# Optimization experiments

Hardware: AMD Instinct MI355X
Metric: run time of the kernel (lower is better)

The kernel has to match this reference:

```python
import jax, jax.numpy as jnp
import numpy as np

B, N, D, C, NCLS = 8, 2048, 256, 128, 50
EPS = 1e-5  # BatchNorm eps

def _bn(x, g, b):
    # eval-mode BatchNorm1d over channel dim of (B,C,N): running_mean=0, running_var=1
    return x * (g / jnp.sqrt(1.0 + EPS))[:, None] + b[:, None]

def _complex_linear(x, Wr, br, Wi, bi):
    # torch ComplexLinear: complex(fr(x.real)-fi(x.imag), fr(x.imag)+fi(x.real))
    xr, xi = x.real, x.imag
    re = (xr @ Wr.T + br) - (xi @ Wi.T + bi)
    im = (xi @ Wr.T + br) + (xr @ Wi.T + bi)
    return jax.lax.complex(re, im)

def _sa(x, qkW, vW, vb, tW, tb, g, b):
    # x: (B,C,N); q/k share weights (tied in torch), dim C//4
    xq = jnp.einsum('qc,bcn->bnq', qkW, x)            # (B,N,C/4)
    xk = jnp.einsum('qc,bcm->bqm', qkW, x)            # (B,C/4,N)
    energy = jnp.einsum('bnq,bqm->bnm', xq, xk)       # (B,N,N)
    attn = jax.nn.softmax(energy, axis=-1)
    attn = attn / (1e-9 + attn.sum(axis=1, keepdims=True))  # column renorm
    xv = jnp.einsum('oc,bcn->bon', vW, x) + vb[:, None]
    xr = x - jnp.einsum('bcn,bnm->bcm', xv, attn)
    xr = jnp.einsum('oc,bcn->bon', tW, xr) + tb[:, None]
    return x + jax.nn.relu(_bn(xr, g, b))

def reference(xyz, cls_label, A, Bmat, W1r, b1r, W1i, b1i, W2r, b2r, W2i, b2i,
              lbl_emb, ft_w1, ft_g1, ft_b1, ft_w2, ft_g2, ft_b2,
              sa_qk, sa_vw, sa_vb, sa_tw, sa_tb, sa_g, sa_b,
              fuse_w, fuse_g, fuse_b, c1_w, c1_b, bn1_g, bn1_b, c2_w, c2_b):
    pts = xyz.transpose(0, 2, 1)                       # (B,N,3)
    # VecKM(d=256, alpha=30, beta=9): G = eB (eB^H eA), normalized to sqrt(d)
    eA = jnp.exp(1j * (pts @ A))                       # (B,N,D) complex64
    eB = jnp.exp(1j * (pts @ Bmat))
    inner = jnp.einsum('bnd,bne->bde', eB.conj(), eA)  # (B,D,D)
    G = jnp.einsum('bnd,bde->bne', eB, inner)          # (B,N,D)
    G = G / jnp.linalg.norm(G, axis=-1, keepdims=True) * jnp.sqrt(jnp.float32(D))
    G = _complex_linear(G, W1r, b1r, W1i, b1i)
    G = jax.lax.complex(jax.nn.relu(G.real), jax.nn.relu(G.imag))  # ComplexReLU
    G = _complex_linear(G, W2r, b2r, W2i, b2i)
    G = (G.real ** 2 + G.imag ** 2).transpose(0, 2, 1)  # (B,D,N)
    reweight = (cls_label @ lbl_emb)[:, :, None]        # (B,D,1)
    x = G * reweight
    x = jax.nn.relu(_bn(jnp.einsum('oc,bcn->bon', ft_w1, x), ft_g1, ft_b1))
    x = _bn(jnp.einsum('oc,bcn->bon', ft_w2, x), ft_g2, ft_b2)  # (B,C,N)
    feats = []
    for i in range(4):
        x = _sa(x, sa_qk[i], sa_vw[i], sa_vb[i], sa_tw[i], sa_tb[i], sa_g[i], sa_b[i])
        feats.append(x)
    x = jnp.concatenate(feats, axis=1)                  # (B,4C,N)
    x = jax.nn.relu(_bn(jnp.einsum('oc,bcn->bon', fuse_w, x), fuse_g, fuse_b))
    x = jax.nn.relu(_bn(jnp.einsum('oc,bcn->bon', c1_w, x) + c1_b[:, None], bn1_g, bn1_b))
    # dropout is identity in eval mode
    x = jnp.einsum('oc,bcn->bon', c2_w, x) + c2_b[:, None]
    x = jax.nn.log_softmax(x, axis=1)
    return x.transpose(0, 2, 1)                         # (B,N,NCLS)

def setup_inputs():
    key = jax.random.key(0)
    k = jax.random.split(key, 24)
    rn = lambda i, s: jax.random.normal(k[i], s, jnp.float32)
    s = 0.05
    return {
        'xyz': rn(0, (B, 3, N)),
        'cls_label': jax.random.uniform(k[1], (B, 16), jnp.float32),
        'A': rn(2, (3, D)) * 30.0,
        'Bmat': rn(3, (3, D)) * 9.0,
        'W1r': rn(4, (D, D)) * s, 'b1r': rn(5, (D,)) * s,
        'W1i': rn(6, (D, D)) * s, 'b1i': rn(7, (D,)) * s,
        'W2r': rn(8, (D, D)) * s, 'b2r': rn(9, (D,)) * s,
        'W2i': rn(10, (D, D)) * s, 'b2i': rn(11, (D,)) * s,
        'lbl_emb': rn(12, (16, D)),
        'ft_w1': rn(13, (C, D)) * s, 'ft_g1': jnp.ones((C,)), 'ft_b1': jnp.zeros((C,)),
        'ft_w2': rn(14, (C, C)) * s, 'ft_g2': jnp.ones((C,)), 'ft_b2': jnp.zeros((C,)),
        'sa_qk': rn(15, (4, C // 4, C)) * s,
        'sa_vw': rn(16, (4, C, C)) * s, 'sa_vb': rn(17, (4, C)) * s,
        'sa_tw': rn(18, (4, C, C)) * s, 'sa_tb': rn(19, (4, C)) * s,
        'sa_g': jnp.ones((4, C)), 'sa_b': jnp.zeros((4, C)),
        'fuse_w': rn(20, (C, 4 * C)) * s, 'fuse_g': jnp.ones((C,)), 'fuse_b': jnp.zeros((C,)),
        'c1_w': rn(21, (C, C)) * s, 'c1_b': rn(22, (C,)) * s,
        'bn1_g': jnp.ones((C,)), 'bn1_b': jnp.zeros((C,)),
        'c2_w': rn(23, (NCLS, C)) * s, 'c2_b': jnp.zeros((NCLS,)),
    }
```

## Files before the change

### kernel.cpp

```cpp
#include <hip/hip_runtime.h>

#define BB 8
#define NPTS 2048
#define DD 256
#define CCH 128
#define NCLASS 50
#define LOG2E 1.4426950408889634f

typedef __attribute__((ext_vector_type(8))) short short8;
typedef __attribute__((ext_vector_type(4))) float f32x4;
typedef unsigned short u16;
#define MFMA16(a,b,c) __builtin_amdgcn_mfma_f32_16x16x32_bf16(a,b,c,0,0,0)

__device__ __forceinline__ u16 f2bf(float x){
  union { float f; unsigned int u; } v; v.f = x;
  unsigned int r = v.u + 0x7FFFu + ((v.u >> 16) & 1u);
  return (u16)(r >> 16);
}
__device__ __forceinline__ float bf2f(u16 u){
  union { unsigned int u32; float f; } v; v.u32 = ((unsigned int)u) << 16; return v.f;
}
__device__ __forceinline__ void split2(float x, u16& h, u16& l){
  h = f2bf(x); l = f2bf(x - bf2f(h));
}
__device__ __forceinline__ short8 ld8(const u16* p){ return *(const short8*)p; }
__device__ __forceinline__ short8 zero8(){ short8 z = {0,0,0,0,0,0,0,0}; return z; }

struct WSplit {
  const float* src[12];
  int cnt[12];
  int off[12];
};
__global__ __launch_bounds__(256) void wsplit_kernel(WSplit wsp, u16* __restrict__ H,
                                                     u16* __restrict__ L)
{
  int seg = blockIdx.y;
  int idx = blockIdx.x*256 + threadIdx.x;
  if (idx >= wsp.cnt[seg]) return;
  float v = wsp.src[seg][idx];
  u16 h, l; split2(v, h, l);
  H[wsp.off[seg]+idx] = h; L[wsp.off[seg]+idx] = l;
}

__global__ __launch_bounds__(256) void ek1_kernel(
    const float* __restrict__ xyz, const float* __restrict__ A, const float* __restrict__ Bm,
    u16* __restrict__ ATrh, u16* __restrict__ ATrl, u16* __restrict__ ATih, u16* __restrict__ ATil,
    u16* __restrict__ BTrh, u16* __restrict__ BTrl, u16* __restrict__ BTih, u16* __restrict__ BTil)
{
  size_t idx = (size_t)blockIdx.x*256 + threadIdx.x;
  int n = (int)(idx & (NPTS-1));
  int d = (int)((idx >> 11) & (DD-1));
  int b = (int)(idx >> 19);
  float p0 = xyz[((size_t)b*3+0)*NPTS+n];
  float p1 = xyz[((size_t)b*3+1)*NPTS+n];
  float p2 = xyz[((size_t)b*3+2)*NPTS+n];
  float phA = p0*A[d] + p1*A[DD+d] + p2*A[2*DD+d];
  float phB = p0*Bm[d] + p1*Bm[DD+d] + p2*Bm[2*DD+d];
  float sa, ca, sb, cb;
  sincosf(phA, &sa, &ca);
  sincosf(phB, &sb, &cb);
  size_t off = ((size_t)b*DD + d)*NPTS + n;
  u16 h, l;
  split2(ca, h, l); ATrh[off] = h; ATrl[off] = l;
  split2(sa, h, l); ATih[off] = h; ATil[off] = l;
  split2(cb, h, l); BTrh[off] = h; BTrl[off] = l;
  split2(sb, h, l); BTih[off] = h; BTil[off] = l;
}

__global__ __launch_bounds__(256) void ek2_kernel(
    const float* __restrict__ xyz, const float* __restrict__ Bm,
    u16* __restrict__ Brh, u16* __restrict__ Brl, u16* __restrict__ Bih, u16* __restrict__ Bil)
{
  size_t idx = (size_t)blockIdx.x*256 + threadIdx.x;
  int d = (int)(idx & (DD-1));
  int n = (int)((idx >> 8) & (NPTS-1));
  int b = (int)(idx >> 19);
  float p0 = xyz[((size_t)b*3+0)*NPTS+n];
  float p1 = xyz[((size_t)b*3+1)*NPTS+n];
  float p2 = xyz[((size_t)b*3+2)*NPTS+n];
  float phB = p0*Bm[d] + p1*Bm[DD+d] + p2*Bm[2*DD+d];
  float sb, cb;
  sincosf(phB, &sb, &cb);
  size_t off = ((size_t)b*NPTS + n)*DD + d;
  u16 h, l;
  split2(cb, h, l); Brh[off] = h; Brl[off] = l;
  split2(sb, h, l); Bih[off] = h; Bil[off] = l;
}

__global__ __launch_bounds__(256) void inner_mfma_kernel(
    const u16* __restrict__ ATrh, const u16* __restrict__ ATrl,
    const u16* __restrict__ ATih, const u16* __restrict__ ATil,
    const u16* __restrict__ BTrh, const u16* __restrict__ BTrl,
    const u16* __restrict__ BTih, const u16* __restrict__ BTil,
    float2* __restrict__ PART)
{
  int z = blockIdx.z; int b = z & 7; int ch = z >> 3;
  int e0 = blockIdx.y*64, d0 = blockIdx.x*64;
  int tid = threadIdx.x, lane = tid & 63, w = tid >> 6;
  int wr = (w >> 1)*32, wc = (w & 1)*32;
  int r16 = lane & 15, g4 = lane >> 4;
  f32x4 re[2][2] = {}, ip[2][2] = {}, iq[2][2] = {};
  size_t ar_[2], br_[2];
  #pragma unroll
  for (int rg = 0; rg < 2; rg++) {
    ar_[rg] = ((size_t)b*DD + (e0 + wr + rg*16 + r16))*NPTS + g4*8;
    br_[rg] = ((size_t)b*DD + (d0 + wc + rg*16 + r16))*NPTS + g4*8;
  }
  int kbeg = ch*512;
  #pragma unroll 2
  for (int kk = 0; kk < 512; kk += 32) {
    int k0 = kbeg + kk;
    short8 arh[2], arl[2], aih[2], ail[2], brh[2], brl[2], bih[2], bil[2];
    #pragma unroll
    for (int rg = 0; rg < 2; rg++) {
      arh[rg] = ld8(ATrh + ar_[rg] + k0); arl[rg] = ld8(ATrl + ar_[rg] + k0);
      aih[rg] = ld8(ATih + ar_[rg] + k0); ail[rg] = ld8(ATil + ar_[rg] + k0);
      brh[rg] = ld8(BTrh + br_[rg] + k0); brl[rg] = ld8(BTrl + br_[rg] + k0);
      bih[rg] = ld8(BTih + br_[rg] + k0); bil[rg] = ld8(BTil + br_[rg] + k0);
    }
    #pragma unroll
    for (int ra = 0; ra < 2; ra++)
      #pragma unroll
      for (int rb = 0; rb < 2; rb++) {
        re[ra][rb] = MFMA16(arh[ra], brh[rb], re[ra][rb]);
        re[ra][rb] = MFMA16(arh[ra], brl[rb], re[ra][rb]);
        re[ra][rb] = MFMA16(arl[ra], brh[rb], re[ra][rb]);
        re[ra][rb] = MFMA16(aih[ra], bih[rb], re[ra][rb]);
        re[ra][rb] = MFMA16(aih[ra], bil[rb], re[ra][rb]);
        re[ra][rb] = MFMA16(ail[ra], bih[rb], re[ra][rb]);
        ip[ra][rb] = MFMA16(aih[ra], brh[rb], ip[ra][rb]);
        ip[ra][rb] = MFMA16(aih[ra], brl[rb], ip[ra][rb]);
        ip[ra][rb] = MFMA16(ail[ra], brh[rb], ip[ra][rb]);
        iq[ra][rb] = MFMA16(arh[ra], bih[rb], iq[ra][rb]);
        iq[ra][rb] = MFMA16(arh[ra], bil[rb], iq[ra][rb]);
        iq[ra][rb] = MFMA16(arl[ra], bih[rb], iq[ra][rb]);
      }
  }
  float2* outp = PART + ((size_t)(ch*BB + b)*DD)*DD;
  #pragma unroll
  for (int ra = 0; ra < 2; ra++)
    #pragma unroll
    for (int rb = 0; rb < 2; rb++)
      #pragma unroll
      for (int j = 0; j < 4; j++) {
        int e = e0 + wr + ra*16 + g4*4 + j;
        int d = d0 + wc + rb*16 + r16;
        outp[(size_t)e*DD + d] = make_float2(re[ra][rb][j], ip[ra][rb][j] - iq[ra][rb][j]);
      }
}

__global__ __launch_bounds__(256) void innred_kernel(const float2* __restrict__ P,
    u16* __restrict__ Irh, u16* __restrict__ Irl, u16* __restrict__ Iih, u16* __restrict__ Iil)
{
  size_t i = (size_t)blockIdx.x*256 + threadIdx.x;
  const size_t S = (size_t)BB*DD*DD;
  float2 a = P[i], b = P[i+S], c = P[i+2*S], d = P[i+3*S];
  float rr = a.x+b.x+c.x+d.x, ii = a.y+b.y+c.y+d.y;
  u16 h, l;
  split2(rr, h, l); Irh[i] = h; Irl[i] = l;
  split2(ii, h, l); Iih[i] = h; Iil[i] = l;
}

__global__ __launch_bounds__(256) void g_mfma_kernel(
    const u16* __restrict__ Brh, const u16* __restrict__ Brl,
    const u16* __restrict__ Bih, const u16* __restrict__ Bil,
    const u16* __restrict__ Irh, const u16* __restrict__ Irl,
    const u16* __restrict__ Iih, const u16* __restrict__ Iil,
    float2* __restrict__ G)
{
  int b = blockIdx.z;
  int n0 = blockIdx.y*64, e0 = blockIdx.x*64;
  int tid = threadIdx.x, lane = tid & 63, w = tid >> 6;
  int wr = (w >> 1)*32, wc = (w & 1)*32;
  int r16 = lane & 15, g4 = lane >> 4;
  f32x4 p[2][2] = {}, q[2][2] = {}, im[2][2] = {};
  size_t ar_[2], br_[2];
  #pragma unroll
  for (int rg = 0; rg < 2; rg++) {
    ar_[rg] = ((size_t)b*NPTS + (n0 + wr + rg*16 + r16))*DD + g4*8;
    br_[rg] = ((size_t)b*DD + (e0 + wc + rg*16 + r16))*DD + g4*8;
  }
  #pragma unroll
  for (int k0 = 0; k0 < DD; k0 += 32) {
    short8 arh[2], arl[2], aih[2], ail[2], brh[2], brl[2], bih[2], bil[2];
    #pragma unroll
    for (int rg = 0; rg < 2; rg++) {
      arh[rg] = ld8(Brh + ar_[rg] + k0); arl[rg] = ld8(Brl + ar_[rg] + k0);
      aih[rg] = ld8(Bih + ar_[rg] + k0); ail[rg] = ld8(Bil + ar_[rg] + k0);
      brh[rg] = ld8(Irh + br_[rg] + k0); brl[rg] = ld8(Irl + br_[rg] + k0);
      bih[rg] = ld8(Iih + br_[rg] + k0); bil[rg] = ld8(Iil + br_[rg] + k0);
    }
    #pragma unroll
    for (int ra = 0; ra < 2; ra++)
      #pragma unroll
      for (int rb = 0; rb < 2; rb++) {
        p[ra][rb] = MFMA16(arh[ra], brh[rb], p[ra][rb]);
        p[ra][rb] = MFMA16(arh[ra], brl[rb], p[ra][rb]);
        p[ra][rb] = MFMA16(arl[ra], brh[rb], p[ra][rb]);
        q[ra][rb] = MFMA16(aih[ra], bih[rb], q[ra][rb]);
        q[ra][rb] = MFMA16(aih[ra], bil[rb], q[ra][rb]);
        q[ra][rb] = MFMA16(ail[ra], bih[rb], q[ra][rb]);
        im[ra][rb] = MFMA16(arh[ra], bih[rb], im[ra][rb]);
        im[ra][rb] = MFMA16(arh[ra], bil[rb], im[ra][rb]);
        im[ra][rb] = MFMA16(arl[ra], bih[rb], im[ra][rb]);
        im[ra][rb] = MFMA16(aih[ra], brh[rb], im[ra][rb]);
        im[ra][rb] = MFMA16(aih[ra], brl[rb], im[ra][rb]);
        im[ra][rb] = MFMA16(ail[ra], brh[rb], im[ra][rb]);
      }
  }
  #pragma unroll
  for (int ra = 0; ra < 2; ra++)
    #pragma unroll
    for (int rb = 0; rb < 2; rb++)
      #pragma unroll
      for (int j = 0; j < 4; j++) {
        int n = n0 + wr + ra*16 + g4*4 + j;
        int e = e0 + wc + rb*16 + r16;
        G[((size_t)b*NPTS + n)*DD + e] = make_float2(p[ra][rb][j] - q[ra][rb][j], im[ra][rb][j]);
      }
}

__global__ __launch_bounds__(256) void gnormsplit_kernel(const float2* __restrict__ Gf,
    u16* __restrict__ Grh, u16* __restrict__ Grl, u16* __restrict__ Gih, u16* __restrict__ Gil)
{
  size_t row = blockIdx.x;
  const float2* p = Gf + row*DD;
  int tid = threadIdx.x;
  float2 v = p[tid];
  __shared__ float red[256];
  red[tid] = v.x*v.x + v.y*v.y;
  __syncthreads();
  for (int w = 128; w > 0; w >>= 1) { if (tid < w) red[tid] += red[tid+w]; __syncthreads(); }
  float sc = 16.f * rsqrtf(red[0]);
  size_t off = row*DD + tid;
  u16 h, l;
  split2(v.x*sc, h, l); Grh[off] = h; Grl[off] = l;
  split2(v.y*sc, h, l); Gih[off] = h; Gil[off] = l;
}

__global__ __launch_bounds__(256) void clinear_mfma_kernel(
    const u16* __restrict__ Arh, const u16* __restrict__ Arl,
    const u16* __restrict__ Aih, const u16* __restrict__ Ail,
    const u16* __restrict__ Wrh, const u16* __restrict__ Wrl,
    const u16* __restrict__ Wih, const u16* __restrict__ Wil,
    const float* __restrict__ br, const float* __restrict__ bi,
    u16* __restrict__ Orh, u16* __restrict__ Orl, u16* __restrict__ Oih, u16* __restrict__ Oil,
    const float* __restrict__ RW, float* __restrict__ GSQ, int mode)
{
  int wg = blockIdx.y * gridDim.x + blockIdx.x;
  int xcd = wg & 7, idx = wg >> 3;
  int o0 = (idx & 3) * 64;
  int m0 = (xcd * ((int)gridDim.y >> 3) + (idx >> 2)) * 64;
  int tid = threadIdx.x, lane = tid & 63, w = tid >> 6;
  int wr = (w >> 1)*32, wc = (w & 1)*32;
  int r16 = lane & 15, g4 = lane >> 4;
  f32x4 p[2][2] = {}, q[2][2] = {}, im[2][2] = {};
  size_t ar_[2], br_[2];
  #pragma unroll
  for (int rg = 0; rg < 2; rg++) {
    ar_[rg] = (size_t)(m0 + wr + rg*16 + r16)*DD + g4*8;
    br_[rg] = (size_t)(o0 + wc + rg*16 + r16)*DD + g4*8;
  }
  #pragma unroll
  for (int k0 = 0; k0 < DD; k0 += 32) {
    short8 arh[2], arl[2], aih[2], ail[2], brh[2], brl[2], bih[2], bil[2];
    #pragma unroll
    for (int rg = 0; rg < 2; rg++) {
      arh[rg] = ld8(Arh + ar_[rg] + k0); arl[rg] = ld8(Arl + ar_[rg] + k0);
      aih[rg] = ld8(Aih + ar_[rg] + k0); ail[rg] = ld8(Ail + ar_[rg] + k0);
      brh[rg] = ld8(Wrh + br_[rg] + k0); brl[rg] = ld8(Wrl + br_[rg] + k0);
      bih[rg] = ld8(Wih + br_[rg] + k0); bil[rg] = ld8(Wil + br_[rg] + k0);
    }
    #pragma unroll
    for (int ra = 0; ra < 2; ra++)
      #pragma unroll
      for (int rb = 0; rb < 2; rb++) {
        p[ra][rb] = MFMA16(arh[ra], brh[rb], p[ra][rb]);
        p[ra][rb] = MFMA16(arh[ra], brl[rb], p[ra][rb]);
        p[ra][rb] = MFMA16(arl[ra], brh[rb], p[ra][rb]);
        q[ra][rb] = MFMA16(aih[ra], bih[rb], q[ra][rb]);
        q[ra][rb] = MFMA16(aih[ra], bil[rb], q[ra][rb]);
        q[ra][rb] = MFMA16(ail[ra], bih[rb], q[ra][rb]);
        im[ra][rb] = MFMA16(arh[ra], bih[rb], im[ra][rb]);
        im[ra][rb] = MFMA16(arh[ra], bil[rb], im[ra][rb]);
        im[ra][rb] = MFMA16(arl[ra], bih[rb], im[ra][rb]);
        im[ra][rb] = MFMA16(aih[ra], brh[rb], im[ra][rb]);
        im[ra][rb] = MFMA16(aih[ra], brl[rb], im[ra][rb]);
        im[ra][rb] = MFMA16(ail[ra], brh[rb], im[ra][rb]);
      }
  }
  #pragma unroll
  for (int ra = 0; ra < 2; ra++)
    #pragma unroll
    for (int rb = 0; rb < 2; rb++) {
      int o = o0 + wc + rb*16 + r16;
      float brv = br[o], biv = bi[o];
      if (mode == 1) {
        #pragma unroll
        for (int j = 0; j < 4; j++) {
          int m = m0 + wr + ra*16 + g4*4 + j;
          float re = fmaxf(p[ra][rb][j] - q[ra][rb][j] + brv - biv, 0.f);
          float iv = fmaxf(im[ra][rb][j] + brv + biv, 0.f);
          size_t off = (size_t)m*DD + o;
          u16 h, l;
          split2(re, h, l); Orh[off] = h; Orl[off] = l;
          split2(iv, h, l); Oih[off] = h; Oil[off] = l;
        }
      } else {
        int mbase = m0 + wr + ra*16 + g4*4;
        int b = mbase >> 11, nb = mbase & (NPTS-1);
        float rwv = RW[(size_t)b*DD + o];
        float4 gv;
        #pragma unroll
        for (int j = 0; j < 4; j++) {
          float re = p[ra][rb][j] - q[ra][rb][j] + brv - biv;
          float iv = im[ra][rb][j] + brv + biv;
          ((float*)&gv)[j] = (re*re + iv*iv) * rwv;
        }
        *(float4*)(GSQ + ((size_t)b*DD + o)*NPTS + nb) = gv;
      }
    }
}

__global__ void rw_kernel(const float* __restrict__ cls, const float* __restrict__ lbl,
                          float* __restrict__ RW)
{
  int b = blockIdx.x; int d = threadIdx.x;
  float s = 0.f;
  #pragma unroll
  for (int k = 0; k < 16; k++) s += cls[b*16+k] * lbl[k*DD+d];
  RW[b*DD+d] = s;
}

__global__ __launch_bounds__(256) void sgemm_kernel(
    const u16* __restrict__ Wh, const u16* __restrict__ Wl,
    const float* __restrict__ X, float* __restrict__ Y,
    const float* __restrict__ RES,
    const float* __restrict__ bias, const float* __restrict__ bng, const float* __restrict__ bnb,
    u16* __restrict__ YBh, u16* __restrict__ YBl, int ybmode,
    int O, int Cin, size_t xbs, size_t ybs, size_t rbs, int flags)
{
  int b = blockIdx.z;
  int n0 = blockIdx.x*64, o0 = blockIdx.y*64;
  const float* x = X + (size_t)b*xbs;
  __shared__ u16 sXh[64][40], sXl[64][40];
  int tid = threadIdx.x, lane = tid & 63, w = tid >> 6;
  int wo = (w >> 1)*32, wn = (w & 1)*32;
  int r16 = lane & 15, g4 = lane >> 4;
  f32x4 acc[2][2] = {};
  int stc = tid >> 3;
  int stn = (tid & 7)*8;
  for (int k0 = 0; k0 < Cin; k0 += 32) {
    const float* px = x + (size_t)(k0+stc)*NPTS + n0 + stn;
    float4 u0 = *(const float4*)px;
    float4 u1 = *(const float4*)(px+4);
    float v[8] = {u0.x,u0.y,u0.z,u0.w,u1.x,u1.y,u1.z,u1.w};
    __syncthreads();
    #pragma unroll
    for (int j = 0; j < 8; j++) {
      u16 h, l; split2(v[j], h, l);
      sXh[stn+j][stc] = h; sXl[stn+j][stc] = l;
    }
    __syncthreads();
    short8 awh[2], awl[2], bxh[2], bxl[2];
    #pragma unroll
    for (int rg = 0; rg < 2; rg++) {
      int orow = o0 + wo + rg*16 + r16;
      if (orow < O) {
        size_t woff = (size_t)orow*Cin + k0 + g4*8;
        awh[rg] = ld8(Wh + woff); awl[rg] = ld8(Wl + woff);
      } else { awh[rg] = zero8(); awl[rg] = zero8(); }
      bxh[rg] = ld8(&sXh[wn + rg*16 + r16][g4*8]);
      bxl[rg] = ld8(&sXl[wn + rg*16 + r16][g4*8]);
    }
    #pragma unroll
    for (int ra = 0; ra < 2; ra++)
      #pragma unroll
      for (int rb = 0; rb < 2; rb++) {
        acc[ra][rb] = MFMA16(awh[ra], bxh[rb], acc[ra][rb]);
        acc[ra][rb] = MFMA16(awh[ra], bxl[rb], acc[ra][rb]);
        acc[ra][rb] = MFMA16(awl[ra], bxh[rb], acc[ra][rb]);
      }
  }
  #pragma unroll
  for (int ra = 0; ra < 2; ra++)
    #pragma unroll
    for (int rb = 0; rb < 2; rb++)
      #pragma unroll
      for (int j = 0; j < 4; j++) {
        int o = o0 + wo + ra*16 + g4*4 + j;
        if (o >= O) continue;
        int n = n0 + wn + rb*16 + r16;
        float v = acc[ra][rb][j];
        if (flags & 1) v += bias[o];
        if (flags & 2) v = v * (bng[o] * rsqrtf(1.f + 1e-5f)) + bnb[o];
        if (flags & 4) v = fmaxf(v, 0.f);
        if (flags & 8) v += RES[(size_t)b*rbs + (size_t)o*NPTS + n];
        if (ybmode == 0) Y[(size_t)b*ybs + (size_t)o*NPTS + n] = v;
        else if (ybmode == 1) YBh[(size_t)b*ybs + (size_t)o*NPTS + n] = f2bf(v);
        else {
          u16 h, l; split2(v, h, l);
          size_t off = ((size_t)b*NPTS + n)*32 + o;
          YBh[off] = h; YBl[off] = l;
        }
      }
}

__global__ __launch_bounds__(256) void sastat_kernel(
    const u16* __restrict__ Qh, const u16* __restrict__ Ql,
    float* __restrict__ PM, float* __restrict__ PS)
{
  int b = blockIdx.z, ch = blockIdx.y;
  int n0 = blockIdx.x*64;
  size_t base = (size_t)b*NPTS*32;
  int tid = threadIdx.x, lane = tid & 63, wid = tid >> 6;
  int r16 = lane & 15, g4 = lane >> 4;
  size_t ao = base + (size_t)(n0 + wid*16 + r16)*32 + g4*8;
  short8 ah = ld8(Qh + ao), al = ld8(Ql + ao);
  float pm[4] = {-3.4e38f,-3.4e38f,-3.4e38f,-3.4e38f};
  float ps[4] = {0.f,0.f,0.f,0.f};
  int mbeg = ch*512, mend = mbeg + 512;
  for (int mt = mbeg; mt < mend; mt += 32) {
    size_t bo0 = base + (size_t)(mt + r16)*32 + g4*8;
    size_t bo1 = bo0 + 16*32;
    short8 bh0 = ld8(Qh+bo0), bl0 = ld8(Ql+bo0);
    short8 bh1 = ld8(Qh+bo1), bl1 = ld8(Ql+bo1);
    f32x4 a0 = {}, a1 = {};
    a0 = MFMA16(ah, bh0, a0); a0 = MFMA16(ah, bl0, a0); a0 = MFMA16(al, bh0, a0);
    a1 = MFMA16(ah, bh1, a1); a1 = MFMA16(ah, bl1, a1); a1 = MFMA16(al, bh1, a1);
    #pragma unroll
    for (int j = 0; j < 4; j++) {
      float v = fmaxf(a0[j], a1[j]);
      float mn = fmaxf(pm[j], v);
      ps[j] = ps[j]*exp2f((pm[j]-mn)*LOG2E)
            + exp2f((a0[j]-mn)*LOG2E) + exp2f((a1[j]-mn)*LOG2E);
      pm[j] = mn;
    }
  }
  #pragma unroll
  for (int j = 0; j < 4; j++) {
    float m = pm[j], s = ps[j];
    #pragma unroll
    for (int d = 1; d < 16; d <<= 1) {
      float om = __shfl_xor(m, d);
      float os = __shfl_xor(s, d);
      float mn = fmaxf(m, om);
      s = s*exp2f((m-mn)*LOG2E) + os*exp2f((om-mn)*LOG2E);
      m = mn;
    }
    if (r16 == 0) {
      int n_ = n0 + wid*16 + g4*4 + j;
      size_t off = ((size_t)ch*BB + b)*NPTS + n_;
      PM[off] = m; PS[off] = s;
    }
  }
}

__global__ __launch_bounds__(256) void comb1_kernel(
    const float* __restrict__ PM, const float* __restrict__ PS,
    float* __restrict__ MX, float* __restrict__ RS)
{
  size_t i = (size_t)blockIdx.x*256 + threadIdx.x;
  const size_t S = (size_t)BB*NPTS;
  float m0 = PM[i], m1 = PM[i+S], m2 = PM[i+2*S], m3 = PM[i+3*S];
  float mx = fmaxf(fmaxf(m0,m1), fmaxf(m2,m3));
  float den = PS[i]*exp2f((m0-mx)*LOG2E) + PS[i+S]*exp2f((m1-mx)*LOG2E)
            + PS[i+2*S]*exp2f((m2-mx)*LOG2E) + PS[i+3*S]*exp2f((m3-mx)*LOG2E);
  MX[i] = mx; RS[i] = 1.f/den;
}

__global__ __launch_bounds__(512) void fused_pv_kernel(
    const u16* __restrict__ Qh, const u16* __restrict__ Ql,
    const float* __restrict__ MX, const float* __restrict__ RS,
    const u16* __restrict__ XV, const float* __restrict__ XRES, size_t res_bs,
    float* __restrict__ OUT)
{
  int b = blockIdx.y;
  int m0 = blockIdx.x*64;
  size_t qbase = (size_t)b*NPTS*32;
  const u16* xv = XV + (size_t)b*CCH*NPTS;
  __shared__ float smx[NPTS], srs[NPTS];
  __shared__ u16 Pl[64][36];
  __shared__ float csacc[64];
  int tid = threadIdx.x, lane = tid & 63, w = tid >> 6;
  int r16 = lane & 15, g4 = lane >> 4;
  for (int t = tid; t < NPTS; t += 512) {
    smx[t] = MX[(size_t)b*NPTS + t];
    srs[t] = RS[(size_t)b*NPTS + t];
  }
  if (tid < 64) csacc[tid] = 0.f;
  int ma = w >> 1, na = w & 1;
  int cw = (w >> 1)*32, mw = (w & 1)*32;
  size_t eao = qbase + (size_t)(m0 + ma*16 + r16)*32 + g4*8;
  short8 eah = ld8(Qh + eao), eal = ld8(Ql + eao);
  const u16* pa0 = xv + (size_t)(cw + r16)*NPTS + g4*8;
  const u16* pa1 = pa0 + (size_t)16*NPTS;
  f32x4 acc[2][2] = {};
  float cs[4] = {0.f,0.f,0.f,0.f};
  size_t ebo = qbase + (size_t)(na*16 + r16)*32 + g4*8;
  short8 ebh = ld8(Qh + ebo), ebl = ld8(Ql + ebo);
  short8 xa0 = ld8(pa0), xa1 = ld8(pa1);
  __syncthreads();
  for (int nt = 0; nt < NPTS; nt += 32) {
    f32x4 e = {};
    e = MFMA16(eah, ebh, e); e = MFMA16(eah, ebl, e); e = MFMA16(eal, ebh, e);
    int nn = nt + na*16 + r16;
    float mxv_ = smx[nn], rsv_ = srs[nn];
    #pragma unroll
    for (int j = 0; j < 4; j++) {
      float t = exp2f((e[j]-mxv_)*LOG2E)*rsv_;
      cs[j] += t;
      Pl[ma*16 + g4*4 + j][na*16 + r16] = f2bf(t);
    }
    short8 nebh = zero8(), nebl = zero8(), nxa0 = zero8(), nxa1 = zero8();
    if (nt + 32 < NPTS) {
      size_t ebo2 = qbase + (size_t)(nt + 32 + na*16 + r16)*32 + g4*8;
      nebh = ld8(Qh + ebo2); nebl = ld8(Ql + ebo2);
      nxa0 = ld8(pa0 + nt + 32); nxa1 = ld8(pa1 + nt + 32);
    }
    __syncthreads();
    short8 b0 = *(const short8*)&Pl[mw + r16][g4*8];
    short8 b1 = *(const short8*)&Pl[mw + 16 + r16][g4*8];
    acc[0][0] = MFMA16(xa0, b0, acc[0][0]);
    acc[0][1] = MFMA16(xa0, b1, acc[0][1]);
    acc[1][0] = MFMA16(xa1, b0, acc[1][0]);
    acc[1][1] = MFMA16(xa1, b1, acc[1][1]);
    __syncthreads();
    ebh = nebh; ebl = nebl; xa0 = nxa0; xa1 = nxa1;
  }
  #pragma unroll
  for (int j = 0; j < 4; j++) {
    float c = cs[j];
    #pragma unroll
    for (int d = 1; d < 16; d <<= 1) c += __shfl_xor(c, d);
    if (r16 == 0) atomicAdd(&csacc[ma*16 + g4*4 + j], c);
  }
  __syncthreads();
  #pragma unroll
  for (int ca = 0; ca < 2; ca++)
    #pragma unroll
    for (int mb = 0; mb < 2; mb++) {
      int m = m0 + mw + mb*16 + r16;
      float ci = 1.f/(1e-9f + csacc[mw + mb*16 + r16]);
      #pragma unroll
      for (int j = 0; j < 4; j++) {
        int c = cw + ca*16 + g4*4 + j;
        float v = XRES[(size_t)b*res_bs + (size_t)c*NPTS + m] - acc[ca][mb][j]*ci;
        OUT[((size_t)b*CCH + c)*NPTS + m] = v;
      }
    }
}

__global__ __launch_bounds__(256) void lsm_kernel(const float* __restrict__ Y,
                                                  float* __restrict__ OUT)
{
  int idx = blockIdx.x*256 + threadIdx.x;
  int b = idx >> 11, n = idx & (NPTS-1);
  const float* p = Y + (size_t)b*NCLASS*NPTS + n;
  float m = -3.4e38f;
  #pragma unroll
  for (int k = 0; k < NCLASS; k++) m = fmaxf(m, p[(size_t)k*NPTS]);
  float s = 0.f;
  #pragma unroll
  for (int k = 0; k < NCLASS; k++) s += expf(p[(size_t)k*NPTS] - m);
  float L = m + logf(s);
  float* o = OUT + (size_t)idx*NCLASS;
  #pragma unroll
  for (int k = 0; k < NCLASS; k++) o[k] = p[(size_t)k*NPTS] - L;
}

extern "C" void kernel_launch(void* const* d_in, const int* in_sizes, int n_in,
                              void* d_out, int out_size, void* d_ws, size_t ws_size,
                              hipStream_t stream)
{
  (void)in_sizes; (void)n_in; (void)out_size; (void)ws_size;
  const float* xyz  = (const float*)d_in[0];
  const float* cls  = (const float*)d_in[1];
  const float* Amat = (const float*)d_in[2];
  const float* Bm   = (const float*)d_in[3];
  const float* W1r  = (const float*)d_in[4];
  const float* b1r  = (const float*)d_in[5];
  const float* W1i  = (const float*)d_in[6];
  const float* b1i  = (const float*)d_in[7];
  const float* W2r  = (const float*)d_in[8];
  const float* b2r  = (const float*)d_in[9];
  const float* W2i  = (const float*)d_in[10];
  const float* b2i  = (const float*)d_in[11];
  const float* lbl  = (const float*)d_in[12];
  const float* ftw1 = (const float*)d_in[13];
  const float* ftg1 = (const float*)d_in[14];
  const float* ftb1 = (const float*)d_in[15];
  const float* ftw2 = (const float*)d_in[16];
  const float* ftg2 = (const float*)d_in[17];
  const float* ftb2 = (const float*)d_in[18];
  const float* saqk = (const float*)d_in[19];
  const float* savw = (const float*)d_in[20];
  const float* savb = (const float*)d_in[21];
  const float* satw = (const float*)d_in[22];
  const float* satb = (const float*)d_in[23];
  const float* sag  = (const float*)d_in[24];
  const float* sab  = (const float*)d_in[25];
  const float* fusew= (const float*)d_in[26];
  const float* fuseg= (const float*)d_in[27];
  const float* fuseb= (const float*)d_in[28];
  const float* c1w  = (const float*)d_in[29];
  const float* c1b  = (const float*)d_in[30];
  const float* bn1g = (const float*)d_in[31];
  const float* bn1b = (const float*)d_in[32];
  const float* c2w  = (const float*)d_in[33];
  const float* c2b  = (const float*)d_in[34];
  float* out = (float*)d_out;

  float* ws = (float*)d_ws;
  const size_t PS  = (size_t)BB*DD*NPTS;
  const size_t ISZ = (size_t)BB*DD*DD;
  u16* U = (u16*)ws;
  u16 *ATrh = U+0*PS, *ATrl = U+1*PS, *ATih = U+2*PS, *ATil = U+3*PS;
  u16 *BTrh = U+4*PS, *BTrl = U+5*PS, *BTih = U+6*PS, *BTil = U+7*PS;
  u16 *Bnrh = U+8*PS, *Bnrl = U+9*PS, *Bnih = U+10*PS, *Bnil = U+11*PS;
  u16 *Irh = U+12*PS, *Irl = U+12*PS+ISZ, *Iih = U+12*PS+2*ISZ, *Iil = U+12*PS+3*ISZ;
  float* gsq = (float*)(U + 12*PS + 4*ISZ);
  float2* PART = (float2*)gsq;
  float2* Gf = (float2*)ws;
  u16 *G1rh = U+4*PS, *G1rl = U+5*PS, *G1ih = U+6*PS, *G1il = U+7*PS;
  u16 *G2rh = U+8*PS, *G2rl = U+9*PS, *G2ih = U+10*PS, *G2il = U+11*PS;
  size_t p = (size_t)BB*NPTS*NPTS;
  float* xfeat = ws + p;  p += (size_t)BB*CCH*NPTS;
  float* feats = ws + p;  p += (size_t)BB*4*CCH*NPTS;
  float* xt1   = ws + p;  p += (size_t)BB*CCH*NPTS;
  float* xt2   = ws + p;  p += (size_t)BB*CCH*NPTS;
  float* ybuf  = ws + p;  p += (size_t)BB*NCLASS*NPTS;
  float* rwb   = ws + p;  p += (size_t)BB*DD;
  float* mxv   = ws + p;  p += (size_t)BB*NPTS;
  float* rsv   = ws + p;  p += (size_t)BB*NPTS;
  float* PMb   = ws + p;  p += (size_t)4*BB*NPTS;
  float* PSb   = ws + p;  p += (size_t)4*BB*NPTS;
  u16* xqh = (u16*)(ws + p);
  u16* xql = xqh + (size_t)BB*NPTS*32;
  u16* xvb = xql + (size_t)BB*NPTS*32;
  u16* wpH = xvb + (size_t)BB*CCH*NPTS;
  u16* wpL = wpH + 557056;

  const int o_w1r=0, o_w1i=65536, o_w2r=131072, o_w2i=196608, o_ft1=262144,
            o_ft2=294912, o_qk=311296, o_vw=327680, o_tw=393216, o_fu=458752,
            o_c1=524288, o_c2=540672;
  WSplit wsp;
  const float* srcs[12] = {W1r,W1i,W2r,W2i,ftw1,ftw2,saqk,savw,satw,fusew,c1w,c2w};
  const int cnts[12] = {65536,65536,65536,65536,32768,16384,16384,65536,65536,65536,16384,6400};
  const int offs[12] = {o_w1r,o_w1i,o_w2r,o_w2i,o_ft1,o_ft2,o_qk,o_vw,o_tw,o_fu,o_c1,o_c2};
  for (int i = 0; i < 12; i++) { wsp.src[i]=srcs[i]; wsp.cnt[i]=cnts[i]; wsp.off[i]=offs[i]; }

  wsplit_kernel<<<dim3(256, 12), 256, 0, stream>>>(wsp, wpH, wpL);
  rw_kernel<<<BB, DD, 0, stream>>>(cls, lbl, rwb);
  ek1_kernel<<<(int)(PS/256), 256, 0, stream>>>(xyz, Amat, Bm,
      ATrh, ATrl, ATih, ATil, BTrh, BTrl, BTih, BTil);
  ek2_kernel<<<(int)(PS/256), 256, 0, stream>>>(xyz, Bm, Bnrh, Bnrl, Bnih, Bnil);
  inner_mfma_kernel<<<dim3(DD/64, DD/64, BB*4), 256, 0, stream>>>(
      ATrh, ATrl, ATih, ATil, BTrh, BTrl, BTih, BTil, PART);
  innred_kernel<<<(int)(ISZ/256), 256, 0, stream>>>(PART, Irh, Irl, Iih, Iil);
  g_mfma_kernel<<<dim3(DD/64, NPTS/64, BB), 256, 0, stream>>>(
      Bnrh, Bnrl, Bnih, Bnil, Irh, Irl, Iih, Iil, Gf);
  gnormsplit_kernel<<<BB*NPTS, 256, 0, stream>>>(Gf, G1rh, G1rl, G1ih, G1il);
  clinear_mfma_kernel<<<dim3(DD/64, (BB*NPTS)/64), 256, 0, stream>>>(
      G1rh, G1rl, G1ih, G1il, wpH+o_w1r, wpL+o_w1r, wpH+o_w1i, wpL+o_w1i,
      b1r, b1i, G2rh, G2rl, G2ih, G2il, nullptr, nullptr, 1);
  clinear_mfma_kernel<<<dim3(DD/64, (BB*NPTS)/64), 256, 0, stream>>>(
      G2rh, G2rl, G2ih, G2il, wpH+o_w2r, wpL+o_w2r, wpH+o_w2i, wpL+o_w2i,
      b2r, b2i, nullptr, nullptr, nullptr, nullptr, rwb, gsq, 2);

  sgemm_kernel<<<dim3(NPTS/64, CCH/64, BB), 256, 0, stream>>>(
      wpH+o_ft1, wpL+o_ft1, gsq, xt1, nullptr, nullptr, ftg1, ftb1, nullptr, nullptr, 0,
      CCH, DD, (size_t)DD*NPTS, (size_t)CCH*NPTS, 0, 2|4);
  sgemm_kernel<<<dim3(NPTS/64, CCH/64, BB), 256, 0, stream>>>(
      wpH+o_ft2, wpL+o_ft2, xt1, xfeat, nullptr, nullptr, ftg2, ftb2, nullptr, nullptr, 0,
      CCH, CCH, (size_t)CCH*NPTS, (size_t)CCH*NPTS, 0, 2);

  const float* xsrc = xfeat;
  size_t xbs = (size_t)CCH*NPTS;
  for (int i = 0; i < 4; i++) {
    sgemm_kernel<<<dim3(NPTS/64, 1, BB), 256, 0, stream>>>(
        wpH+o_qk + i*32*CCH, wpL+o_qk + i*32*CCH, xsrc, nullptr, nullptr,
        nullptr, nullptr, nullptr, xqh, xql, 2, 32, CCH, xbs, 0, 0, 0);
    sastat_kernel<<<dim3(NPTS/64, 4, BB), 256, 0, stream>>>(xqh, xql, PMb, PSb);
    comb1_kernel<<<(BB*NPTS)/256, 256, 0, stream>>>(PMb, PSb, mxv, rsv);
    sgemm_kernel<<<dim3(NPTS/64, CCH/64, BB), 256, 0, stream>>>(
        wpH+o_vw + i*CCH*CCH, wpL+o_vw + i*CCH*CCH, xsrc, nullptr, nullptr,
        savb + i*CCH, nullptr, nullptr, xvb, nullptr, 1, CCH, CCH, xbs,
        (size_t)CCH*NPTS, 0, 1);
    fused_pv_kernel<<<dim3(NPTS/64, BB), 512, 0, stream>>>(
        xqh, xql, mxv, rsv, xvb, xsrc, xbs, xt2);
    sgemm_kernel<<<dim3(NPTS/64, CCH/64, BB), 256, 0, stream>>>(
        wpH+o_tw + i*CCH*CCH, wpL+o_tw + i*CCH*CCH, xt2, feats + (size_t)i*CCH*NPTS, xsrc,
        satb + i*CCH, sag + i*CCH, sab + i*CCH, nullptr, nullptr, 0,
        CCH, CCH, (size_t)CCH*NPTS, (size_t)4*CCH*NPTS, xbs, 1|2|4|8);
    xsrc = feats + (size_t)i*CCH*NPTS;
    xbs = (size_t)4*CCH*NPTS;
  }

  sgemm_kernel<<<dim3(NPTS/64, CCH/64, BB), 256, 0, stream>>>(
      wpH+o_fu, wpL+o_fu, feats, xt1, nullptr, nullptr, fuseg, fuseb, nullptr, nullptr, 0,
      CCH, 4*CCH, (size_t)4*CCH*NPTS, (size_t)CCH*NPTS, 0, 2|4);
  sgemm_kernel<<<dim3(NPTS/64, CCH/64, BB), 256, 0, stream>>>(
      wpH+o_c1, wpL+o_c1, xt1, xt2, nullptr, c1b, bn1g, bn1b, nullptr, nullptr, 0,
      CCH, CCH, (size_t)CCH*NPTS, (size_t)CCH*NPTS, 0, 1|2|4);
  sgemm_kernel<<<dim3(NPTS/64, 1, BB), 256, 0, stream>>>(
      wpH+o_c2, wpL+o_c2, xt2, ybuf, nullptr, c2b, nullptr, nullptr, nullptr, nullptr, 0,
      NCLASS, CCH, (size_t)CCH*NPTS, (size_t)NCLASS*NPTS, 0, 1);
  lsm_kernel<<<(BB*NPTS)/256, 256, 0, stream>>>(ybuf, out);
}
```

Baseline: 970.5 us.

## Fuse softmax partial combine into PV kernel, widen PV tile, simplify clinear grid

Removes the separate comb1 kernel by combining the four partial softmax max/sum values inside fused_pv_kernel's shared-memory preload, which saves a launch and a global round trip per SA layer. The PV inner loop now handles 64 keys per iteration instead of 32, halving the number of barriers, but it drops the register prefetch of the next Q and V tiles, so loads are issued in the same iteration that consumes them. The clinear kernel also loses its XCD-aware block swizzle in favour of plain blockIdx mapping, which may reduce L2 locality. Each PV block now recomputes the combine work that comb1 did once.

```diff
diff --git a/kernel.cpp b/kernel.cpp
--- a/kernel.cpp
+++ b/kernel.cpp
@@ -247,10 +247,7 @@
     u16* __restrict__ Orh, u16* __restrict__ Orl, u16* __restrict__ Oih, u16* __restrict__ Oil,
     const float* __restrict__ RW, float* __restrict__ GSQ, int mode)
 {
-  int wg = blockIdx.y * gridDim.x + blockIdx.x;
-  int xcd = wg & 7, idx = wg >> 3;
-  int o0 = (idx & 3) * 64;
-  int m0 = (xcd * ((int)gridDim.y >> 3) + (idx >> 2)) * 64;
+  int m0 = blockIdx.y*64, o0 = blockIdx.x*64;
   int tid = threadIdx.x, lane = tid & 63, w = tid >> 6;
   int wr = (w >> 1)*32, wc = (w & 1)*32;
   int r16 = lane & 15, g4 = lane >> 4;
@@ -456,22 +453,9 @@
   }
 }
 
-__global__ __launch_bounds__(256) void comb1_kernel(
-    const float* __restrict__ PM, const float* __restrict__ PS,
-    float* __restrict__ MX, float* __restrict__ RS)
-{
-  size_t i = (size_t)blockIdx.x*256 + threadIdx.x;
-  const size_t S = (size_t)BB*NPTS;
-  float m0 = PM[i], m1 = PM[i+S], m2 = PM[i+2*S], m3 = PM[i+3*S];
-  float mx = fmaxf(fmaxf(m0,m1), fmaxf(m2,m3));
-  float den = PS[i]*exp2f((m0-mx)*LOG2E) + PS[i+S]*exp2f((m1-mx)*LOG2E)
-            + PS[i+2*S]*exp2f((m2-mx)*LOG2E) + PS[i+3*S]*exp2f((m3-mx)*LOG2E);
-  MX[i] = mx; RS[i] = 1.f/den;
-}
-
 __global__ __launch_bounds__(512) void fused_pv_kernel(
     const u16* __restrict__ Qh, const u16* __restrict__ Ql,
-    const float* __restrict__ MX, const float* __restrict__ RS,
+    const float* __restrict__ PM, const float* __restrict__ PS,
     const u16* __restrict__ XV, const float* __restrict__ XRES, size_t res_bs,
     float* __restrict__ OUT)
 {
@@ -480,13 +464,18 @@
   size_t qbase = (size_t)b*NPTS*32;
   const u16* xv = XV + (size_t)b*CCH*NPTS;
   __shared__ float smx[NPTS], srs[NPTS];
-  __shared__ u16 Pl[64][36];
+  __shared__ u16 Pl[64][72];
   __shared__ float csacc[64];
   int tid = threadIdx.x, lane = tid & 63, w = tid >> 6;
   int r16 = lane & 15, g4 = lane >> 4;
+  const size_t S = (size_t)BB*NPTS;
   for (int t = tid; t < NPTS; t += 512) {
-    smx[t] = MX[(size_t)b*NPTS + t];
-    srs[t] = RS[(size_t)b*NPTS + t];
+    size_t bn = (size_t)b*NPTS + t;
+    float m0_ = PM[bn], m1 = PM[S+bn], m2 = PM[2*S+bn], m3 = PM[3*S+bn];
+    float mxv = fmaxf(fmaxf(m0_,m1), fmaxf(m2,m3));
+    float den = PS[bn]*exp2f((m0_-mxv)*LOG2E) + PS[S+bn]*exp2f((m1-mxv)*LOG2E)
+              + PS[2*S+bn]*exp2f((m2-mxv)*LOG2E) + PS[3*S+bn]*exp2f((m3-mxv)*LOG2E);
+    smx[t] = mxv; srs[t] = 1.f/den;
   }
   if (tid < 64) csacc[tid] = 0.f;
   int ma = w >> 1, na = w & 1;
@@ -497,36 +486,40 @@
   const u16* pa1 = pa0 + (size_t)16*NPTS;
   f32x4 acc[2][2] = {};
   float cs[4] = {0.f,0.f,0.f,0.f};
-  size_t ebo = qbase + (size_t)(na*16 + r16)*32 + g4*8;
-  short8 ebh = ld8(Qh + ebo), ebl = ld8(Ql + ebo);
-  short8 xa0 = ld8(pa0), xa1 = ld8(pa1);
   __syncthreads();
-  for (int nt = 0; nt < NPTS; nt += 32) {
-    f32x4 e = {};
-    e = MFMA16(eah, ebh, e); e = MFMA16(eah, ebl, e); e = MFMA16(eal, ebh, e);
-    int nn = nt + na*16 + r16;
-    float mxv_ = smx[nn], rsv_ = srs[nn];
-    #pragma unroll
-    for (int j = 0; j < 4; j++) {
-      float t = exp2f((e[j]-mxv_)*LOG2E)*rsv_;
-      cs[j] += t;
-      Pl[ma*16 + g4*4 + j][na*16 + r16] = f2bf(t);
-    }
-    short8 nebh = zero8(), nebl = zero8(), nxa0 = zero8(), nxa1 = zero8();
-    if (nt + 32 < NPTS) {
-      size_t ebo2 = qbase + (size_t)(nt + 32 + na*16 + r16)*32 + g4*8;
-      nebh = ld8(Qh + ebo2); nebl = ld8(Ql + ebo2);
-      nxa0 = ld8(pa0 + nt + 32); nxa1 = ld8(pa1 + nt + 32);
+  for (int nt = 0; nt < NPTS; nt += 64) {
+    #pragma unroll
+    for (int sub = 0; sub < 2; sub++) {
+      int nc = nt + na*32 + sub*16;
+      size_t ebo = qbase + (size_t)(nc + r16)*32 + g4*8;
+      short8 ebh = ld8(Qh + ebo), ebl = ld8(Ql + ebo);
+      f32x4 e = {};
+      e = MFMA16(eah, ebh, e); e = MFMA16(eah, ebl, e); e = MFMA16(eal, ebh, e);
+      int nn = nc + r16;
+      float mxv_ = smx[nn], rsv_ = srs[nn];
+      #pragma unroll
+      for (int j = 0; j < 4; j++) {
+        float t = exp2f((e[j]-mxv_)*LOG2E)*rsv_;
+        cs[j] += t;
+        Pl[ma*16 + g4*4 + j][na*32 + sub*16 + r16] = f2bf(t);
+      }
     }
     __syncthreads();
-    short8 b0 = *(const short8*)&Pl[mw + r16][g4*8];
-    short8 b1 = *(const short8*)&Pl[mw + 16 + r16][g4*8];
-    acc[0][0] = MFMA16(xa0, b0, acc[0][0]);
-    acc[0][1] = MFMA16(xa0, b1, acc[0][1]);
-    acc[1][0] = MFMA16(xa1, b0, acc[1][0]);
-    acc[1][1] = MFMA16(xa1, b1, acc[1][1]);
+    short8 xa0 = ld8(pa0 + nt), xa1 = ld8(pa1 + nt);
+    short8 xb0 = ld8(pa0 + nt + 32), xb1 = ld8(pa1 + nt + 32);
+    short8 p0  = *(const short8*)&Pl[mw + r16][g4*8];
+    short8 p1  = *(const short8*)&Pl[mw + 16 + r16][g4*8];
+    short8 p0b = *(const short8*)&Pl[mw + r16][32 + g4*8];
+    short8 p1b = *(const short8*)&Pl[mw + 16 + r16][32 + g4*8];
+    acc[0][0] = MFMA16(xa0, p0, acc[0][0]);
+    acc[0][1] = MFMA16(xa0, p1, acc[0][1]);
+    acc[1][0] = MFMA16(xa1, p0, acc[1][0]);
+    acc[1][1] = MFMA16(xa1, p1, acc[1][1]);
+    acc[0][0] = MFMA16(xb0, p0b, acc[0][0]);
+    acc[0][1] = MFMA16(xb0, p1b, acc[0][1]);
+    acc[1][0] = MFMA16(xb1, p0b, acc[1][0]);
+    acc[1][1] = MFMA16(xb1, p1b, acc[1][1]);
     __syncthreads();
-    ebh = nebh; ebl = nebl; xa0 = nxa0; xa1 = nxa1;
   }
   #pragma unroll
   for (int j = 0; j < 4; j++) {
@@ -631,8 +624,6 @@
   float* xt2   = ws + p;  p += (size_t)BB*CCH*NPTS;
   float* ybuf  = ws + p;  p += (size_t)BB*NCLASS*NPTS;
   float* rwb   = ws + p;  p += (size_t)BB*DD;
-  float* mxv   = ws + p;  p += (size_t)BB*NPTS;
-  float* rsv   = ws + p;  p += (size_t)BB*NPTS;
   float* PMb   = ws + p;  p += (size_t)4*BB*NPTS;
   float* PSb   = ws + p;  p += (size_t)4*BB*NPTS;
   u16* xqh = (u16*)(ws + p);
@@ -682,13 +673,12 @@
         wpH+o_qk + i*32*CCH, wpL+o_qk + i*32*CCH, xsrc, nullptr, nullptr,
         nullptr, nullptr, nullptr, xqh, xql, 2, 32, CCH, xbs, 0, 0, 0);
     sastat_kernel<<<dim3(NPTS/64, 4, BB), 256, 0, stream>>>(xqh, xql, PMb, PSb);
-    comb1_kernel<<<(BB*NPTS)/256, 256, 0, stream>>>(PMb, PSb, mxv, rsv);
     sgemm_kernel<<<dim3(NPTS/64, CCH/64, BB), 256, 0, stream>>>(
         wpH+o_vw + i*CCH*CCH, wpL+o_vw + i*CCH*CCH, xsrc, nullptr, nullptr,
         savb + i*CCH, nullptr, nullptr, xvb, nullptr, 1, CCH, CCH, xbs,
         (size_t)CCH*NPTS, 0, 1);
     fused_pv_kernel<<<dim3(NPTS/64, BB), 512, 0, stream>>>(
-        xqh, xql, mxv, rsv, xvb, xsrc, xbs, xt2);
+        xqh, xql, PMb, PSb, xvb, xsrc, xbs, xt2);
     sgemm_kernel<<<dim3(NPTS/64, CCH/64, BB), 256, 0, stream>>>(
         wpH+o_tw + i*CCH*CCH, wpL+o_tw + i*CCH*CCH, xt2, feats + (size_t)i*CCH*NPTS, xsrc,
         satb + i*CCH, sag + i*CCH, sab + i*CCH, nullptr, nullptr, 0,
```

Measured after the change: 963.4 us. No clear change (-0.7%).
